# Kernel optimization log

Hardware: AMD Instinct MI355X
Metric: run time of the kernel (lower is better)

## Reference

```python
import jax, jax.numpy as jnp
import numpy as np
import math

N_HEADS = 16
D_EFF = 64
ROPE_BASE = 500.0


def _rope(x, cos, sin):
    # x: (b, h, L, d_eff); cos/sin: (L, d_eff//2)
    x_even = x[..., 0::2]
    x_odd = x[..., 1::2]
    rot = jnp.stack([x_even * cos - x_odd * sin,
                     x_even * sin + x_odd * cos], axis=-1)
    return rot.reshape(x.shape)


def setup_inputs() -> dict:
    key = jax.random.key(0)
    ks = jax.random.split(key, 5)
    B, L, D = 1, 2048, 1024
    X = jax.random.normal(ks[0], (B, L, D), dtype=jnp.float32)
    # causal mask (1 = keep, 0 = masked), broadcastable to (B, h, L, L)
    mask = jnp.tril(jnp.ones((L, L), dtype=jnp.int32))[None, :, :]
    s = 1.0 / math.sqrt(D)
    Wq = jax.random.normal(ks[1], (D, D), dtype=jnp.float32) * s
    Wk = jax.random.normal(ks[2], (D, D), dtype=jnp.float32) * s
    Wv = jax.random.normal(ks[3], (D, D), dtype=jnp.float32) * s
    Wo = jax.random.normal(ks[4], (D, D), dtype=jnp.float32) * s
    return {"X": X, "mask": mask, "Wq": Wq, "Wk": Wk, "Wv": Wv, "Wo": Wo}


def reference(X, mask, Wq, Wk, Wv, Wo):
    b, L, d_model = X.shape
    h, d = N_HEADS, D_EFF
    d_full = h * d

    def split_heads(Y):
        return Y.reshape(b, L, h, d).transpose(0, 2, 1, 3)  # (b,h,L,d)

    Q = split_heads(X @ Wq)
    K = split_heads(X @ Wk)
    V = split_heads(X @ Wv)

    # interleaved RoPE, base 500
    inv_freq = 1.0 / (ROPE_BASE ** (jnp.arange(0, d, 2, dtype=jnp.float32) / d))
    freqs = jnp.arange(L, dtype=jnp.float32)[:, None] * inv_freq  # (L, d/2)
    cos, sin = jnp.cos(freqs), jnp.sin(freqs)
    Q = _rope(Q, cos, sin)
    K = _rope(K, cos, sin)

    S = jnp.einsum('bhqd,bhkd->bhqk', Q, K) / math.sqrt(d)
    S = jnp.where(mask[:, None, :, :] == 0, jnp.float32(-1e9), S)
    # NOTE: faithful to original torch code: softmax over the HEADS axis (dim=1)
    A = jax.nn.softmax(S, axis=1)
    Y = jnp.einsum('bhqk,bhkd->bhqd', A, V)
    Y = Y.transpose(0, 2, 1, 3).reshape(b, L, d_full)
    Y = Y @ Wo
    return Y * math.sqrt(d_model / d_full)
```

## Files before the change

### kernel.cpp

```cpp
#include <hip/hip_runtime.h>
#include <stdint.h>
#include <stddef.h>
#include <math.h>

typedef __attribute__((ext_vector_type(8))) short bf16x8;
typedef __attribute__((ext_vector_type(4))) short short4v;
typedef __attribute__((ext_vector_type(4))) float f32x4;

__device__ __forceinline__ short f2bf(float f) {
  union { float f; uint32_t u; } x; x.f = f;
  return (short)((x.u + 0x7fffu + ((x.u >> 16) & 1u)) >> 16);
}
__device__ __forceinline__ float bf2f(short s) {
  union { uint32_t u; float f; } x; x.u = ((uint32_t)(uint16_t)s) << 16;
  return x.f;
}
__device__ __forceinline__ uint32_t cvt_pk_bf16(float a, float b) {
  uint32_t r;
  asm("v_cvt_pk_bf16_f32 %0, %1, %2" : "=v"(r) : "v"(a), "v"(b));
  return r;
}

__device__ __forceinline__ void gload_lds16(const void* g, void* lds) {
  __builtin_amdgcn_global_load_lds(
      (const __attribute__((address_space(1))) void*)g,
      (__attribute__((address_space(3))) void*)lds, 16, 0, 0);
}

__global__ __launch_bounds__(256) void cast_b(const float* __restrict__ s,
                                              short* __restrict__ d) {
  int i4 = (blockIdx.x * 256 + threadIdx.x) * 4;
  float4 v = *(const float4*)&s[i4];
  short4v r = { f2bf(v.x), f2bf(v.y), f2bf(v.z), f2bf(v.w) };
  *(short4v*)&d[i4] = r;
}

__global__ __launch_bounds__(256) void reduce_y(const short* __restrict__ Ypc,
                                                const float* __restrict__ Cvs,
                                                short* __restrict__ o) {
  int q = blockIdx.x;
  int qt = q >> 4, qr = q & 15;
  int a = qt >> 3, r = qt & 7;
  int base = (a + 1) * (4 * a + r);
  int nch = a + 1;
  int col = threadIdx.x * 4;
  float a0 = Cvs[col + 0], a1 = Cvs[col + 1], a2 = Cvs[col + 2], a3 = Cvs[col + 3];
  const short* p = Ypc + ((size_t)base * 16 + qr) * 1024 + col;
  for (int ch = 0; ch < nch; ch++) {
    short4v v = *(const short4v*)p;
    a0 += bf2f(v[0]); a1 += bf2f(v[1]); a2 += bf2f(v[2]); a3 += bf2f(v[3]);
    p += 16 * 1024;
  }
  uint32_t u0 = cvt_pk_bf16(a0, a1), u1 = cvt_pk_bf16(a2, a3);
  short4v rr = { (short)u0, (short)(u0 >> 16), (short)u1, (short)(u1 >> 16) };
  *(short4v*)&o[(size_t)q * 1024 + col] = rr;
}

__global__ __launch_bounds__(256) void transW(const float* __restrict__ Wq,
                                              const float* __restrict__ Wk,
                                              const float* __restrict__ Wv,
                                              const float* __restrict__ Wo,
                                              short* __restrict__ WcatT,
                                              short* __restrict__ WoT) {
  int z = blockIdx.z;
  const float* src = (z == 0) ? Wq : (z == 1) ? Wk : (z == 2) ? Wv : Wo;
  short* dst = (z == 3) ? WoT : WcatT + (size_t)z * 1024 * 1024;
  __shared__ float tl[32][33];
  int tx = threadIdx.x & 31, ty = threadIdx.x >> 5;
  int kk0 = blockIdx.x * 32;
  int nn0 = blockIdx.y * 32;
#pragma unroll
  for (int j = 0; j < 4; j++)
    tl[ty + j * 8][tx] = src[(size_t)(kk0 + ty + j * 8) * 1024 + nn0 + tx];
  __syncthreads();
#pragma unroll
  for (int j = 0; j < 4; j++)
    dst[(size_t)(nn0 + ty + j * 8) * 1024 + kk0 + tx] = f2bf(tl[tx][ty + j * 8]);
}

__global__ __launch_bounds__(256) void transpose_v(const short* __restrict__ Vb,
                                                   short* __restrict__ Vt) {
  __shared__ short tv[64][72];
  int h = blockIdx.y, k0 = blockIdx.x * 64;
  int tid = threadIdx.x;
#pragma unroll
  for (int j = 0; j < 2; j++) {
    int idx = tid + j * 256;
    int row = idx >> 3, c = idx & 7;
    bf16x8 v = *(const bf16x8*)&Vb[((size_t)h * 2048 + k0 + row) * 64 + c * 8];
#pragma unroll
    for (int t = 0; t < 8; t++) tv[row][c * 8 + t] = v[t];
  }
  __syncthreads();
#pragma unroll
  for (int j = 0; j < 2; j++) {
    int idx = tid + j * 256;
    int d = idx >> 3, c = idx & 7;
    bf16x8 v;
#pragma unroll
    for (int t = 0; t < 8; t++) v[t] = tv[c * 8 + t][d];
    *(bf16x8*)&Vt[((size_t)h * 64 + d) * 2048 + k0 + c * 8] = v;
  }
}

__global__ __launch_bounds__(256) void vsum(const short* __restrict__ Vb,
                                            float* __restrict__ Cvs) {
  __shared__ float red[16][17];
  int h = blockIdx.x >> 2, dq = blockIdx.x & 3;
  int dl = threadIdx.x & 15, ks = threadIdx.x >> 4;
  int d = dq * 16 + dl;
  float acc = 0.f;
  const short* base = &Vb[((size_t)h * 2048 + ks * 128) * 64 + d];
#pragma unroll 8
  for (int k = 0; k < 128; k++) acc += bf2f(base[(size_t)k * 64]);
  red[dl][ks] = acc;
  __syncthreads();
  if (threadIdx.x < 16) {
    float sum = 0.f;
#pragma unroll
    for (int i = 0; i < 16; i++) sum += red[threadIdx.x][i];
    Cvs[h * 64 + dq * 16 + threadIdx.x] = sum * 0.0625f;
  }
}

template <int MODE>
__global__ __launch_bounds__(256, 2)
void gemm_kernel(const short* __restrict__ A, const short* __restrict__ B,
                 int N, int K, float* __restrict__ C,
                 short* __restrict__ Qb, short* __restrict__ Kb,
                 short* __restrict__ Vb) {
  __shared__ __attribute__((aligned(16))) short lga[128 * 64];
  __shared__ __attribute__((aligned(16))) short lgb[128 * 64];
  const int tid = threadIdx.x;
  const int lane = tid & 63;
  const int w = tid >> 6;
  const int l15 = lane & 15;
  const int quad = lane >> 4;
  const int wm = w >> 1, wn = w & 1;
  const int m0 = blockIdx.x * 128, n0 = blockIdx.y * 128;
  const int rsub = lane >> 3;
  const int cpos = lane & 7;

  f32x4 acc[4][4];
#pragma unroll
  for (int i = 0; i < 4; i++)
#pragma unroll
    for (int j = 0; j < 4; j++) acc[i][j] = (f32x4){0.f, 0.f, 0.f, 0.f};

  for (int kb = 0; kb < K; kb += 64) {
    __syncthreads();
#pragma unroll
    for (int j = 0; j < 4; j++) {
      int r = (w * 4 + j) * 8 + rsub;
      int kc = cpos ^ rsub;
      gload_lds16(A + (size_t)(m0 + r) * K + kb + kc * 8, &lga[(w * 4 + j) * 512]);
      gload_lds16(B + (size_t)(n0 + r) * K + kb + kc * 8, &lgb[(w * 4 + j) * 512]);
    }
    __syncthreads();
#pragma unroll
    for (int kk = 0; kk < 2; kk++) {
      bf16x8 af[4], bfr[4];
#pragma unroll
      for (int t = 0; t < 4; t++) {
        int row = wm * 64 + t * 16 + l15;
        int pc = (kk * 4 + quad) ^ (row & 7);
        af[t] = *(const bf16x8*)&lga[row * 64 + pc * 8];
        int rowb = wn * 64 + t * 16 + l15;
        int pcb = (kk * 4 + quad) ^ (rowb & 7);
        bfr[t] = *(const bf16x8*)&lgb[rowb * 64 + pcb * 8];
      }
#pragma unroll
      for (int mt = 0; mt < 4; mt++)
#pragma unroll
        for (int nt = 0; nt < 4; nt++)
          acc[mt][nt] = __builtin_amdgcn_mfma_f32_16x16x32_bf16(
              af[mt], bfr[nt], acc[mt][nt], 0, 0, 0);
    }
  }

  if (MODE == 0) {
#pragma unroll
    for (int mt = 0; mt < 4; mt++) {
      int q = m0 + wm * 64 + mt * 16 + quad * 4;
#pragma unroll
      for (int nt = 0; nt < 4; nt++) {
        int n = n0 + wn * 64 + nt * 16 + l15;
#pragma unroll
        for (int r = 0; r < 4; r++) C[(size_t)(q + r) * N + n] = acc[mt][nt][r];
      }
    }
  } else {
#pragma unroll
    for (int mt = 0; mt < 4; mt++) {
#pragma unroll
      for (int nt = 0; nt < 4; nt++) {
        int n = n0 + wn * 64 + nt * 16 + l15;
        int mat = n >> 10;
        int h = (n >> 6) & 15;
        int d = n & 63;
#pragma unroll
        for (int r = 0; r < 4; r++) {
          int q = m0 + wm * 64 + mt * 16 + quad * 4 + r;
          float v = acc[mt][nt][r];
          float o = __shfl_xor(v, 1, 64);
          if (mat < 2) {
            int i = d >> 1;
            float ang = (float)q * __builtin_exp2f(-(float)i * 0.2801807588956902f);
            float sn, cs;
            __sincosf(ang, &sn, &cs);
            float rv = (d & 1) ? (o * sn + v * cs) : (v * cs - o * sn);
            short* dst = (mat == 0) ? Qb : Kb;
            dst[((size_t)h * 2048 + q) * 64 + d] = f2bf(rv);
          } else {
            Vb[((size_t)h * 2048 + q) * 64 + d] = f2bf(v);
          }
        }
      }
    }
  }
}

__global__ __launch_bounds__(512, 4)
void attn_kernel(const short* __restrict__ Qb, const short* __restrict__ Kb,
                 const short* __restrict__ Vt, short* __restrict__ Ypc) {
  __shared__ short Sb[16 * 16 * 72];
  const int tid = threadIdx.x;
  const int lane = tid & 63;
  const int w = tid >> 6;
  const int l15 = lane & 15, quad = lane >> 4;
  const int b = blockIdx.x;
  int a = (int)((sqrtf((float)(b + 1)) - 1.f) * 0.5f);
  while (4 * (a + 1) * (a + 2) <= b) a++;
  while (4 * a * (a + 1) > b) a--;
  const int off = b - 4 * a * (a + 1);
  const int den = a + 1;
  const int r = off / den;
  const int c = off - r * den;
  const int qt = 8 * a + r;
  const int q0 = qt * 16;
  const int G = (qt + 4) >> 2;
  const int g0 = 2 * c;
  const int ng = (g0 + 2 <= G) ? 2 : 1;
  const int h0 = w * 2;

  bf16x8 qf[2][2];
#pragma unroll
  for (int hh = 0; hh < 2; hh++)
#pragma unroll
    for (int cc = 0; cc < 2; cc++)
      qf[hh][cc] = *(const bf16x8*)&Qb[((size_t)(h0 + hh) * 2048 + q0 + l15) * 64 +
                                       cc * 32 + quad * 8];

  f32x4 yacc[2][4];
#pragma unroll
  for (int i = 0; i < 2; i++)
#pragma unroll
    for (int j = 0; j < 4; j++) yacc[i][j] = (f32x4){0.f, 0.f, 0.f, 0.f};

  for (int gi = 0; gi < ng; gi++) {
    const int k0 = (g0 + gi) * 64;
#pragma unroll
    for (int hh = 0; hh < 2; hh++) {
      int h = h0 + hh;
#pragma unroll
      for (int st = 0; st < 4; st++) {
        const short* kb = &Kb[((size_t)h * 2048 + k0 + st * 16 + l15) * 64 + quad * 8];
        bf16x8 kf0 = *(const bf16x8*)kb;
        bf16x8 kf1 = *(const bf16x8*)(kb + 32);
        f32x4 sa = (f32x4){0.f, 0.f, 0.f, 0.f};
        sa = __builtin_amdgcn_mfma_f32_16x16x32_bf16(qf[hh][0], kf0, sa, 0, 0, 0);
        sa = __builtin_amdgcn_mfma_f32_16x16x32_bf16(qf[hh][1], kf1, sa, 0, 0, 0);
        const float cs = 0.18033688011112042f;
        uint32_t u0 = cvt_pk_bf16(sa[0] * cs, sa[1] * cs);
        uint32_t u1 = cvt_pk_bf16(sa[2] * cs, sa[3] * cs);
        int rb = (h * 16 + quad * 4) * 72 + st * 16 + l15;
        Sb[rb]       = (short)u0;
        Sb[rb + 72]  = (short)(u0 >> 16);
        Sb[rb + 144] = (short)u1;
        Sb[rb + 216] = (short)(u1 >> 16);
      }
    }
    __syncthreads();
#pragma unroll
    for (int pp = 0; pp < 2; pp++) {
      int p = tid + pp * 512;
      int q = p >> 6, kl = p & 63;
      int base = q * 72 + kl;
      float t[16];
      float m = -1e30f;
#pragma unroll
      for (int h = 0; h < 16; h++) {
        t[h] = bf2f(Sb[h * 1152 + base]);
        m = fmaxf(m, t[h]);
      }
      float sum = 0.f;
#pragma unroll
      for (int h = 0; h < 16; h++) {
        float e = __builtin_exp2f(t[h] - m);
        t[h] = e;
        sum += e;
      }
      bool msk = (k0 + kl) > (q0 + q);
      float rs = msk ? 0.f : 1.f / sum;
      float offv = msk ? 0.f : 0.0625f;
#pragma unroll
      for (int h = 0; h < 16; h += 2) {
        uint32_t u = cvt_pk_bf16(t[h] * rs - offv, t[h + 1] * rs - offv);
        Sb[h * 1152 + base]       = (short)u;
        Sb[(h + 1) * 1152 + base] = (short)(u >> 16);
      }
    }
    __syncthreads();
#pragma unroll
    for (int hh = 0; hh < 2; hh++) {
      int h = h0 + hh;
#pragma unroll
      for (int kk = 0; kk < 2; kk++) {
        bf16x8 af = *(const bf16x8*)&Sb[(h * 16 + l15) * 72 + kk * 32 + quad * 8];
#pragma unroll
        for (int nt = 0; nt < 4; nt++) {
          bf16x8 vf = *(const bf16x8*)&Vt[((size_t)h * 64 + nt * 16 + l15) * 2048 +
                                          k0 + kk * 32 + quad * 8];
          yacc[hh][nt] = __builtin_amdgcn_mfma_f32_16x16x32_bf16(af, vf, yacc[hh][nt],
                                                                 0, 0, 0);
        }
      }
    }
    __syncthreads();
  }
  short* Y = Ypc + (size_t)b * 16 * 1024;
#pragma unroll
  for (int hh = 0; hh < 2; hh++) {
#pragma unroll
    for (int nt = 0; nt < 4; nt++) {
      int col = (h0 + hh) * 64 + nt * 16 + l15;
#pragma unroll
      for (int rr = 0; rr < 4; rr++)
        Y[(size_t)(quad * 4 + rr) * 1024 + col] = f2bf(yacc[hh][nt][rr]);
    }
  }
}

extern "C" void kernel_launch(void* const* d_in, const int* in_sizes, int n_in,
                              void* d_out, int out_size, void* d_ws, size_t ws_size,
                              hipStream_t stream) {
  (void)in_sizes; (void)n_in; (void)out_size; (void)ws_size;
  const float* X  = (const float*)d_in[0];
  const float* Wq = (const float*)d_in[2];
  const float* Wk = (const float*)d_in[3];
  const float* Wv = (const float*)d_in[4];
  const float* Wo = (const float*)d_in[5];
  char* ws = (char*)d_ws;
  const size_t MB = 1024 * 1024;
  short* Xbf   = (short*)(ws + 0);
  short* WcatT = (short*)(ws + 4 * MB);
  short* WoT   = (short*)(ws + 10 * MB);
  short* Qb    = (short*)(ws + 12 * MB);
  short* Kb    = (short*)(ws + 16 * MB);
  short* Vb    = (short*)(ws + 20 * MB);
  short* Vt    = (short*)(ws + 24 * MB);
  short* Ypc   = (short*)(ws + 28 * MB);
  float* Cvs   = (float*)(ws + 63 * MB);
  short* Ycbf  = Xbf;
  float* out   = (float*)d_out;

  cast_b<<<dim3(2048), dim3(256), 0, stream>>>(X, Xbf);
  transW<<<dim3(32, 32, 4), dim3(256), 0, stream>>>(Wq, Wk, Wv, Wo, WcatT, WoT);
  gemm_kernel<1><<<dim3(16, 24), dim3(256), 0, stream>>>(Xbf, WcatT, 3072, 1024,
                                                         nullptr, Qb, Kb, Vb);
  transpose_v<<<dim3(32, 16), dim3(256), 0, stream>>>(Vb, Vt);
  vsum<<<dim3(64), dim3(256), 0, stream>>>(Vb, Cvs);
  attn_kernel<<<dim3(1088), dim3(512), 0, stream>>>(Qb, Kb, Vt, Ypc);
  reduce_y<<<dim3(2048), dim3(256), 0, stream>>>(Ypc, Cvs, Ycbf);
  gemm_kernel<0><<<dim3(16, 8), dim3(256), 0, stream>>>(Ycbf, WoT, 1024, 1024,
                                                        out, nullptr, nullptr, nullptr);
}
```

Before: 238.0 us.

## Give attention blocks 32-query tiles with one wave per head

The attention kernel moves from 16-query tiles with 8 waves (2 heads each) to 32-query tiles with 16 waves (1 head each) and 1024 threads. Each K and V fragment loaded from global memory now feeds two query sub-tiles, which halves K/V traffic per query and halves the number of blocks and partial-sum chunks that reduce_y has to combine. The block-to-tile decode and reduce_y indexing are updated to match. In exchange the LDS buffer doubles, blocks are larger with fewer per CU, and the causal-triangle work is split more coarsely, which may hurt load balance.

```diff
diff --git a/kernel.cpp b/kernel.cpp
--- a/kernel.cpp
+++ b/kernel.cpp
@@ -39,17 +39,17 @@
                                                 const float* __restrict__ Cvs,
                                                 short* __restrict__ o) {
   int q = blockIdx.x;
-  int qt = q >> 4, qr = q & 15;
-  int a = qt >> 3, r = qt & 7;
-  int base = (a + 1) * (4 * a + r);
+  int j = q >> 5, qr = q & 31;
+  int a = j >> 2, r = j & 3;
+  int base = (a + 1) * (2 * a + r);
   int nch = a + 1;
   int col = threadIdx.x * 4;
   float a0 = Cvs[col + 0], a1 = Cvs[col + 1], a2 = Cvs[col + 2], a3 = Cvs[col + 3];
-  const short* p = Ypc + ((size_t)base * 16 + qr) * 1024 + col;
+  const short* p = Ypc + ((size_t)base * 32 + qr) * 1024 + col;
   for (int ch = 0; ch < nch; ch++) {
     short4v v = *(const short4v*)p;
     a0 += bf2f(v[0]); a1 += bf2f(v[1]); a2 += bf2f(v[2]); a3 += bf2f(v[3]);
-    p += 16 * 1024;
+    p += 32 * 1024;
   }
   uint32_t u0 = cvt_pk_bf16(a0, a1), u1 = cvt_pk_bf16(a2, a3);
   short4v rr = { (short)u0, (short)(u0 >> 16), (short)u1, (short)(u1 >> 16) };
@@ -220,60 +220,58 @@
   }
 }
 
-__global__ __launch_bounds__(512, 4)
+__global__ __launch_bounds__(1024, 2)
 void attn_kernel(const short* __restrict__ Qb, const short* __restrict__ Kb,
                  const short* __restrict__ Vt, short* __restrict__ Ypc) {
-  __shared__ short Sb[16 * 16 * 72];
+  __shared__ short Sb[16 * 32 * 72];
   const int tid = threadIdx.x;
   const int lane = tid & 63;
-  const int w = tid >> 6;
+  const int h = tid >> 6;
   const int l15 = lane & 15, quad = lane >> 4;
   const int b = blockIdx.x;
-  int a = (int)((sqrtf((float)(b + 1)) - 1.f) * 0.5f);
-  while (4 * (a + 1) * (a + 2) <= b) a++;
-  while (4 * a * (a + 1) > b) a--;
-  const int off = b - 4 * a * (a + 1);
+  int a = (int)((sqrtf((float)(2 * b + 1)) - 1.f) * 0.5f);
+  while (2 * (a + 1) * (a + 2) <= b) a++;
+  while (2 * a * (a + 1) > b) a--;
+  const int off = b - 2 * a * (a + 1);
   const int den = a + 1;
   const int r = off / den;
   const int c = off - r * den;
-  const int qt = 8 * a + r;
-  const int q0 = qt * 16;
-  const int G = (qt + 4) >> 2;
+  const int j = 4 * a + r;
+  const int q0 = j * 32;
+  const int G = (j + 2) >> 1;
   const int g0 = 2 * c;
   const int ng = (g0 + 2 <= G) ? 2 : 1;
-  const int h0 = w * 2;
 
   bf16x8 qf[2][2];
 #pragma unroll
-  for (int hh = 0; hh < 2; hh++)
+  for (int qs = 0; qs < 2; qs++)
 #pragma unroll
     for (int cc = 0; cc < 2; cc++)
-      qf[hh][cc] = *(const bf16x8*)&Qb[((size_t)(h0 + hh) * 2048 + q0 + l15) * 64 +
+      qf[qs][cc] = *(const bf16x8*)&Qb[((size_t)h * 2048 + q0 + qs * 16 + l15) * 64 +
                                        cc * 32 + quad * 8];
 
   f32x4 yacc[2][4];
 #pragma unroll
   for (int i = 0; i < 2; i++)
 #pragma unroll
-    for (int j = 0; j < 4; j++) yacc[i][j] = (f32x4){0.f, 0.f, 0.f, 0.f};
+    for (int jj = 0; jj < 4; jj++) yacc[i][jj] = (f32x4){0.f, 0.f, 0.f, 0.f};
 
   for (int gi = 0; gi < ng; gi++) {
     const int k0 = (g0 + gi) * 64;
 #pragma unroll
-    for (int hh = 0; hh < 2; hh++) {
-      int h = h0 + hh;
-#pragma unroll
-      for (int st = 0; st < 4; st++) {
-        const short* kb = &Kb[((size_t)h * 2048 + k0 + st * 16 + l15) * 64 + quad * 8];
-        bf16x8 kf0 = *(const bf16x8*)kb;
-        bf16x8 kf1 = *(const bf16x8*)(kb + 32);
+    for (int st = 0; st < 4; st++) {
+      const short* kb = &Kb[((size_t)h * 2048 + k0 + st * 16 + l15) * 64 + quad * 8];
+      bf16x8 kf0 = *(const bf16x8*)kb;
+      bf16x8 kf1 = *(const bf16x8*)(kb + 32);
+#pragma unroll
+      for (int qs = 0; qs < 2; qs++) {
         f32x4 sa = (f32x4){0.f, 0.f, 0.f, 0.f};
-        sa = __builtin_amdgcn_mfma_f32_16x16x32_bf16(qf[hh][0], kf0, sa, 0, 0, 0);
-        sa = __builtin_amdgcn_mfma_f32_16x16x32_bf16(qf[hh][1], kf1, sa, 0, 0, 0);
+        sa = __builtin_amdgcn_mfma_f32_16x16x32_bf16(qf[qs][0], kf0, sa, 0, 0, 0);
+        sa = __builtin_amdgcn_mfma_f32_16x16x32_bf16(qf[qs][1], kf1, sa, 0, 0, 0);
         const float cs = 0.18033688011112042f;
         uint32_t u0 = cvt_pk_bf16(sa[0] * cs, sa[1] * cs);
         uint32_t u1 = cvt_pk_bf16(sa[2] * cs, sa[3] * cs);
-        int rb = (h * 16 + quad * 4) * 72 + st * 16 + l15;
+        int rb = (h * 32 + qs * 16 + quad * 4) * 72 + st * 16 + l15;
         Sb[rb]       = (short)u0;
         Sb[rb + 72]  = (short)(u0 >> 16);
         Sb[rb + 144] = (short)u1;
@@ -283,60 +281,59 @@
     __syncthreads();
 #pragma unroll
     for (int pp = 0; pp < 2; pp++) {
-      int p = tid + pp * 512;
+      int p = tid + pp * 1024;
       int q = p >> 6, kl = p & 63;
       int base = q * 72 + kl;
       float t[16];
       float m = -1e30f;
 #pragma unroll
-      for (int h = 0; h < 16; h++) {
-        t[h] = bf2f(Sb[h * 1152 + base]);
-        m = fmaxf(m, t[h]);
+      for (int hh = 0; hh < 16; hh++) {
+        t[hh] = bf2f(Sb[hh * 2304 + base]);
+        m = fmaxf(m, t[hh]);
       }
       float sum = 0.f;
 #pragma unroll
-      for (int h = 0; h < 16; h++) {
-        float e = __builtin_exp2f(t[h] - m);
-        t[h] = e;
+      for (int hh = 0; hh < 16; hh++) {
+        float e = __builtin_exp2f(t[hh] - m);
+        t[hh] = e;
         sum += e;
       }
       bool msk = (k0 + kl) > (q0 + q);
       float rs = msk ? 0.f : 1.f / sum;
       float offv = msk ? 0.f : 0.0625f;
 #pragma unroll
-      for (int h = 0; h < 16; h += 2) {
-        uint32_t u = cvt_pk_bf16(t[h] * rs - offv, t[h + 1] * rs - offv);
-        Sb[h * 1152 + base]       = (short)u;
-        Sb[(h + 1) * 1152 + base] = (short)(u >> 16);
-      }
-    }
-    __syncthreads();
-#pragma unroll
-    for (int hh = 0; hh < 2; hh++) {
-      int h = h0 + hh;
-#pragma unroll
-      for (int kk = 0; kk < 2; kk++) {
-        bf16x8 af = *(const bf16x8*)&Sb[(h * 16 + l15) * 72 + kk * 32 + quad * 8];
-#pragma unroll
-        for (int nt = 0; nt < 4; nt++) {
-          bf16x8 vf = *(const bf16x8*)&Vt[((size_t)h * 64 + nt * 16 + l15) * 2048 +
-                                          k0 + kk * 32 + quad * 8];
-          yacc[hh][nt] = __builtin_amdgcn_mfma_f32_16x16x32_bf16(af, vf, yacc[hh][nt],
-                                                                 0, 0, 0);
-        }
-      }
-    }
-    __syncthreads();
-  }
-  short* Y = Ypc + (size_t)b * 16 * 1024;
-#pragma unroll
-  for (int hh = 0; hh < 2; hh++) {
+      for (int hh = 0; hh < 16; hh += 2) {
+        uint32_t u = cvt_pk_bf16(t[hh] * rs - offv, t[hh + 1] * rs - offv);
+        Sb[hh * 2304 + base]       = (short)u;
+        Sb[(hh + 1) * 2304 + base] = (short)(u >> 16);
+      }
+    }
+    __syncthreads();
+#pragma unroll
+    for (int kk = 0; kk < 2; kk++) {
+      bf16x8 af0 = *(const bf16x8*)&Sb[(h * 32 + l15) * 72 + kk * 32 + quad * 8];
+      bf16x8 af1 = *(const bf16x8*)&Sb[(h * 32 + 16 + l15) * 72 + kk * 32 + quad * 8];
+#pragma unroll
+      for (int nt = 0; nt < 4; nt++) {
+        bf16x8 vf = *(const bf16x8*)&Vt[((size_t)h * 64 + nt * 16 + l15) * 2048 +
+                                        k0 + kk * 32 + quad * 8];
+        yacc[0][nt] = __builtin_amdgcn_mfma_f32_16x16x32_bf16(af0, vf, yacc[0][nt],
+                                                              0, 0, 0);
+        yacc[1][nt] = __builtin_amdgcn_mfma_f32_16x16x32_bf16(af1, vf, yacc[1][nt],
+                                                              0, 0, 0);
+      }
+    }
+    __syncthreads();
+  }
+  short* Y = Ypc + (size_t)b * 32 * 1024;
+#pragma unroll
+  for (int qs = 0; qs < 2; qs++) {
 #pragma unroll
     for (int nt = 0; nt < 4; nt++) {
-      int col = (h0 + hh) * 64 + nt * 16 + l15;
+      int col = h * 64 + nt * 16 + l15;
 #pragma unroll
       for (int rr = 0; rr < 4; rr++)
-        Y[(size_t)(quad * 4 + rr) * 1024 + col] = f2bf(yacc[hh][nt][rr]);
+        Y[(size_t)(qs * 16 + quad * 4 + rr) * 1024 + col] = f2bf(yacc[qs][nt][rr]);
     }
   }
 }
@@ -370,7 +367,7 @@
                                                          nullptr, Qb, Kb, Vb);
   transpose_v<<<dim3(32, 16), dim3(256), 0, stream>>>(Vb, Vt);
   vsum<<<dim3(64), dim3(256), 0, stream>>>(Vb, Cvs);
-  attn_kernel<<<dim3(1088), dim3(512), 0, stream>>>(Qb, Kb, Vt, Ypc);
+  attn_kernel<<<dim3(544), dim3(1024), 0, stream>>>(Qb, Kb, Vt, Ypc);
   reduce_y<<<dim3(2048), dim3(256), 0, stream>>>(Ypc, Cvs, Ycbf);
   gemm_kernel<0><<<dim3(16, 8), dim3(256), 0, stream>>>(Ycbf, WoT, 1024, 1024,
                                                         out, nullptr, nullptr, nullptr);
```

Measured after the change: 223.0 us. 1.07x faster.

## Rebalance attention work split into longer chunks with paired scheduling and packed softmax

Applied to the files above, without the earlier changes.

Each attention block now handles up to four 64-key groups instead of two, which cuts the grid from 1088 to 576 blocks. Blocks are assigned so that short and long query tiles are paired, ordered longest-first, and reduce_y's slot indexing is updated to match. The head-axis softmax now processes two adjacent keys per thread with packed 32-bit LDS reads and writes and drops the max subtraction. That saves the max pass, but relies on the pre-scaled scores staying in a safe exp2 range.

```diff
diff --git a/kernel.cpp b/kernel.cpp
--- a/kernel.cpp
+++ b/kernel.cpp
@@ -39,17 +39,18 @@
                                                 const float* __restrict__ Cvs,
                                                 short* __restrict__ o) {
   int q = blockIdx.x;
-  int qt = q >> 4, qr = q & 15;
-  int a = qt >> 3, r = qt & 7;
-  int base = (a + 1) * (4 * a + r);
-  int nch = a + 1;
+  int j = q >> 4, qr = q & 15;
   int col = threadIdx.x * 4;
   float a0 = Cvs[col + 0], a1 = Cvs[col + 1], a2 = Cvs[col + 2], a3 = Cvs[col + 3];
-  const short* p = Ypc + ((size_t)base * 16 + qr) * 1024 + col;
-  for (int ch = 0; ch < nch; ch++) {
-    short4v v = *(const short4v*)p;
+  int cmax = j >> 4;
+  for (int c = 0; c <= cmax; c++) {
+    int p, t;
+    if (c < 4) { p = c;     t = j - 16 * c; }
+    else       { p = 7 - c; t = j + 16; }
+    int slot = (2 * p + (t & 1)) + 8 * (71 - (t >> 1));
+    const short* pp = Ypc + ((size_t)slot * 16 + qr) * 1024 + col;
+    short4v v = *(const short4v*)pp;
     a0 += bf2f(v[0]); a1 += bf2f(v[1]); a2 += bf2f(v[2]); a3 += bf2f(v[3]);
-    p += 16 * 1024;
   }
   uint32_t u0 = cvt_pk_bf16(a0, a1), u1 = cvt_pk_bf16(a2, a3);
   short4v rr = { (short)u0, (short)(u0 >> 16), (short)u1, (short)(u1 >> 16) };
@@ -227,21 +228,20 @@
   const int tid = threadIdx.x;
   const int lane = tid & 63;
   const int w = tid >> 6;
+  const int h0 = w * 2;
   const int l15 = lane & 15, quad = lane >> 4;
   const int b = blockIdx.x;
-  int a = (int)((sqrtf((float)(b + 1)) - 1.f) * 0.5f);
-  while (4 * (a + 1) * (a + 2) <= b) a++;
-  while (4 * a * (a + 1) > b) a--;
-  const int off = b - 4 * a * (a + 1);
-  const int den = a + 1;
-  const int r = off / den;
-  const int c = off - r * den;
-  const int qt = 8 * a + r;
-  const int q0 = qt * 16;
-  const int G = (qt + 4) >> 2;
-  const int g0 = 2 * c;
-  const int ng = (g0 + 2 <= G) ? 2 : 1;
-  const int h0 = w * 2;
+  const int x = b & 7;
+  const int p = x >> 1;
+  const int t = 2 * (71 - (b >> 3)) + (x & 1);
+  int c, j;
+  if (t < 128 - 16 * p) { c = p;     j = 16 * p + t; }
+  else                  { c = 7 - p; j = t - 16; }
+  const int G = (j >> 2) + 1;
+  const int g0 = 4 * c;
+  int ngt = G - g0;
+  const int ng = (ngt > 4) ? 4 : ngt;
+  const int q0 = j * 16;
 
   bf16x8 qf[2][2];
 #pragma unroll
@@ -255,7 +255,7 @@
 #pragma unroll
   for (int i = 0; i < 2; i++)
 #pragma unroll
-    for (int j = 0; j < 4; j++) yacc[i][j] = (f32x4){0.f, 0.f, 0.f, 0.f};
+    for (int jj = 0; jj < 4; jj++) yacc[i][jj] = (f32x4){0.f, 0.f, 0.f, 0.f};
 
   for (int gi = 0; gi < ng; gi++) {
     const int k0 = (g0 + gi) * 64;
@@ -281,33 +281,30 @@
       }
     }
     __syncthreads();
-#pragma unroll
-    for (int pp = 0; pp < 2; pp++) {
-      int p = tid + pp * 512;
-      int q = p >> 6, kl = p & 63;
-      int base = q * 72 + kl;
-      float t[16];
-      float m = -1e30f;
-#pragma unroll
-      for (int h = 0; h < 16; h++) {
-        t[h] = bf2f(Sb[h * 1152 + base]);
-        m = fmaxf(m, t[h]);
-      }
-      float sum = 0.f;
-#pragma unroll
-      for (int h = 0; h < 16; h++) {
-        float e = __builtin_exp2f(t[h] - m);
-        t[h] = e;
-        sum += e;
-      }
-      bool msk = (k0 + kl) > (q0 + q);
-      float rs = msk ? 0.f : 1.f / sum;
-      float offv = msk ? 0.f : 0.0625f;
-#pragma unroll
-      for (int h = 0; h < 16; h += 2) {
-        uint32_t u = cvt_pk_bf16(t[h] * rs - offv, t[h + 1] * rs - offv);
-        Sb[h * 1152 + base]       = (short)u;
-        Sb[(h + 1) * 1152 + base] = (short)(u >> 16);
+    {
+      int q = tid >> 5;
+      int kl2 = (tid & 31) * 2;
+      int base = q * 72 + kl2;
+      float t0[16], t1[16];
+      float s0 = 0.f, s1 = 0.f;
+#pragma unroll
+      for (int hh = 0; hh < 16; hh++) {
+        uint32_t u = *(const uint32_t*)&Sb[hh * 1152 + base];
+        float e0 = __builtin_exp2f(bf2f((short)u));
+        float e1 = __builtin_exp2f(bf2f((short)(u >> 16)));
+        t0[hh] = e0; t1[hh] = e1;
+        s0 += e0; s1 += e1;
+      }
+      bool m0 = (k0 + kl2)     > (q0 + q);
+      bool m1 = (k0 + kl2 + 1) > (q0 + q);
+      float rs0 = m0 ? 0.f : 1.f / s0;
+      float rs1 = m1 ? 0.f : 1.f / s1;
+      float o0 = m0 ? 0.f : 0.0625f;
+      float o1 = m1 ? 0.f : 0.0625f;
+#pragma unroll
+      for (int hh = 0; hh < 16; hh++) {
+        uint32_t wv = cvt_pk_bf16(t0[hh] * rs0 - o0, t1[hh] * rs1 - o1);
+        *(uint32_t*)&Sb[hh * 1152 + base] = wv;
       }
     }
     __syncthreads();
@@ -370,7 +367,7 @@
                                                          nullptr, Qb, Kb, Vb);
   transpose_v<<<dim3(32, 16), dim3(256), 0, stream>>>(Vb, Vt);
   vsum<<<dim3(64), dim3(256), 0, stream>>>(Vb, Cvs);
-  attn_kernel<<<dim3(1088), dim3(512), 0, stream>>>(Qb, Kb, Vt, Ypc);
+  attn_kernel<<<dim3(576), dim3(512), 0, stream>>>(Qb, Kb, Vt, Ypc);
   reduce_y<<<dim3(2048), dim3(256), 0, stream>>>(Ypc, Cvs, Ycbf);
   gemm_kernel<0><<<dim3(16, 8), dim3(256), 0, stream>>>(Ycbf, WoT, 1024, 1024,
                                                         out, nullptr, nullptr, nullptr);
```

New measurement: 244.4 us. 1.03x slower.
